# Kernel optimization log

Hardware: AMD Instinct MI355X
Metric: run time of the kernel (lower is better)

Reference implementation:

```python
import jax, jax.numpy as jnp
import numpy as np

U, N, E, D = 200000, 50000, 1600000, 64


def setup_inputs() -> dict:
    key = jax.random.key(0)
    ks = jax.random.split(key, 8)
    nodes = jax.random.randint(ks[0], (N,), 0, U)
    neigh_idx = jax.random.randint(ks[1], (E,), 0, U)
    seg_ids = jnp.sort(jax.random.randint(ks[2], (E,), 0, N))
    u2e = jax.random.normal(ks[3], (U, D), dtype=jnp.float32) * 0.1
    W1 = jax.random.normal(ks[4], (2 * D, D), dtype=jnp.float32) * 0.1
    b1 = jnp.zeros((D,), dtype=jnp.float32)
    W2 = jax.random.normal(ks[5], (D, D), dtype=jnp.float32) * 0.1
    b2 = jnp.zeros((D,), dtype=jnp.float32)
    w3 = jax.random.normal(ks[6], (D, 1), dtype=jnp.float32) * 0.1
    b3 = jnp.zeros((1,), dtype=jnp.float32)
    return {"nodes": nodes, "neigh_idx": neigh_idx, "seg_ids": seg_ids,
            "u2e": u2e, "W1": W1, "b1": b1, "W2": W2, "b2": b2,
            "w3": w3, "b3": b3}


def reference(nodes, neigh_idx, seg_ids, u2e, W1, b1, W2, b2, w3, b3):
    # Per-node self representation  [N, D]
    u_rep = u2e[nodes]
    # Ragged neighbor gather flattened to edge list
    e_u = u2e[neigh_idx]                      # [E, D]
    u_edge = u_rep[seg_ids]                   # [E, D] node rep broadcast to its edges
    # Attention MLP (GraphRec-style), eval mode (no dropout)
    x = jnp.concatenate([e_u, u_edge], axis=1)            # [E, 2D]
    x = jax.nn.relu(x @ W1 + b1)
    x = jax.nn.relu(x @ W2 + b2)
    logits = (x @ w3 + b3)[:, 0]                           # [E]
    # Segment softmax over each node's neighbor set
    seg_max = jax.ops.segment_max(logits, seg_ids, num_segments=N)
    ex = jnp.exp(logits - seg_max[seg_ids])
    denom = jax.ops.segment_sum(ex, seg_ids, num_segments=N)
    att = ex / denom[seg_ids]                              # [E]
    # Attention-weighted neighbor aggregation: e_u^T @ att per node
    agg = jax.ops.segment_sum(att[:, None] * e_u, seg_ids, num_segments=N)  # [N, D]
    # Nodes with zero neighbors fall back to their own embedding
    counts = jax.ops.segment_sum(jnp.ones((E,), dtype=jnp.float32), seg_ids, num_segments=N)
    out = jnp.where(counts[:, None] > 0, agg, u_rep)
    return out
```

## Files before the change

kernel.cpp:

```cpp
#include <hip/hip_runtime.h>
#include <math.h>

#define D 64

typedef __fp16 fp16x2 __attribute__((ext_vector_type(2)));
typedef _Float16 half8 __attribute__((ext_vector_type(8)));
typedef _Float16 half4v __attribute__((ext_vector_type(4)));
typedef __attribute__((ext_vector_type(4))) float f32x4;

union h8pun { half8 v; fp16x2 h2[4]; };

__global__ __launch_bounds__(256) void k_prep(const float* __restrict__ W1,
                                              const float* __restrict__ W2,
                                              float* __restrict__ W1at,
                                              float* __restrict__ W1bt,
                                              _Float16* __restrict__ W2h,
                                              const int* __restrict__ seg_ids,
                                              int* __restrict__ start, int E, int N) {
    int i = blockIdx.x * 256 + threadIdx.x;
    if (i < 3 * D * D) {
        int mat = i / (D * D), j = i % (D * D);
        if (mat == 0) {
            int r = j >> 6, c = j & 63;
            W1at[c * D + r] = W1[r * D + c];
        } else if (mat == 1) {
            int r = j >> 6, c = j & 63;
            W1bt[c * D + r] = W1[(D + r) * D + c];
        } else {
            int n = j >> 6, pos = j & 63;
            int k = (pos >> 2) + 16 * (pos & 3);
            W2h[n * D + pos] = (_Float16)W2[k * D + n];
        }
    }
    if (i <= N) {
        int lo = 0, hi = E;
        while (lo < hi) {
            int mid = (lo + hi) >> 1;
            if (seg_ids[mid] < i) lo = mid + 1; else hi = mid;
        }
        start[i] = lo;
    }
}

__global__ __launch_bounds__(256) void k_proj_both(const float* __restrict__ u2e,
                                                   const int* __restrict__ nodes,
                                                   const float* __restrict__ W1at,
                                                   const float* __restrict__ W1bt,
                                                   const float* __restrict__ b1,
                                                   _Float16* __restrict__ q,
                                                   _Float16* __restrict__ u2e_h,
                                                   _Float16* __restrict__ p,
                                                   int U, int N, int wavesU, int wavesN) {
    int lane = threadIdx.x & 63;
    int m = lane & 15, quad = lane >> 4;
    int wave = (blockIdx.x * blockDim.x + threadIdx.x) >> 6;

    const float* Wt;
    const int* idx;
    const float* bias;
    _Float16* outp;
    _Float16* copyp;
    int R, w0, wstride;
    if (wave < wavesU) {
        Wt = W1at; idx = nullptr; bias = nullptr; outp = q; copyp = u2e_h;
        R = U; w0 = wave; wstride = wavesU;
    } else {
        Wt = W1bt; idx = nodes; bias = b1; outp = p; copyp = nullptr;
        R = N; w0 = wave - wavesU; wstride = wavesN;
    }

    half8 Bf[2][4];
    float bv[4];
#pragma unroll
    for (int t = 0; t < 4; ++t) {
        int n = m + 16 * t;
        bv[t] = bias ? bias[n] : 0.0f;
#pragma unroll
        for (int kh = 0; kh < 2; ++kh) {
            const float* col = Wt + n * D + kh * 32 + quad * 8;
#pragma unroll
            for (int j = 0; j < 8; ++j) Bf[kh][t][j] = (_Float16)col[j];
        }
    }

    int ngroups = (R + 15) / 16;
    for (int g = w0; g < ngroups; g += wstride) {
        int r_ = g * 16 + m;
        int rs = r_ < R ? r_ : R - 1;
        int src = idx ? idx[rs] : rs;
        const float4* arow = (const float4*)(u2e + (size_t)src * D);
        float4 x0 = arow[quad * 2], x1 = arow[quad * 2 + 1];
        float4 y0 = arow[8 + quad * 2], y1 = arow[8 + quad * 2 + 1];
        h8pun A0, A1;
        A0.h2[0] = __builtin_amdgcn_cvt_pkrtz(x0.x, x0.y);
        A0.h2[1] = __builtin_amdgcn_cvt_pkrtz(x0.z, x0.w);
        A0.h2[2] = __builtin_amdgcn_cvt_pkrtz(x1.x, x1.y);
        A0.h2[3] = __builtin_amdgcn_cvt_pkrtz(x1.z, x1.w);
        A1.h2[0] = __builtin_amdgcn_cvt_pkrtz(y0.x, y0.y);
        A1.h2[1] = __builtin_amdgcn_cvt_pkrtz(y0.z, y0.w);
        A1.h2[2] = __builtin_amdgcn_cvt_pkrtz(y1.x, y1.y);
        A1.h2[3] = __builtin_amdgcn_cvt_pkrtz(y1.z, y1.w);
        if (copyp && r_ < R) {
            *(half8*)(copyp + (size_t)r_ * D + quad * 8) = A0.v;
            *(half8*)(copyp + (size_t)r_ * D + 32 + quad * 8) = A1.v;
        }
        f32x4 C[4];
#pragma unroll
        for (int t = 0; t < 4; ++t) C[t] = (f32x4){bv[t], bv[t], bv[t], bv[t]};
#pragma unroll
        for (int t = 0; t < 4; ++t) {
            C[t] = __builtin_amdgcn_mfma_f32_16x16x32_f16(A0.v, Bf[0][t], C[t], 0, 0, 0);
            C[t] = __builtin_amdgcn_mfma_f32_16x16x32_f16(A1.v, Bf[1][t], C[t], 0, 0, 0);
        }
#pragma unroll
        for (int r = 0; r < 4; ++r) {
            int row = g * 16 + quad * 4 + r;
            if (row < R) {
                half4v hv = {(_Float16)C[0][r], (_Float16)C[1][r],
                             (_Float16)C[2][r], (_Float16)C[3][r]};
                *(half4v*)(outp + (size_t)row * D + m * 4) = hv;
            }
        }
    }
}

__global__ __launch_bounds__(256) void k_edge_ex(const int* __restrict__ neigh_idx,
                                                 const int* __restrict__ seg_ids,
                                                 const _Float16* __restrict__ q,
                                                 const _Float16* __restrict__ p,
                                                 const _Float16* __restrict__ W2h,
                                                 const float* __restrict__ b2,
                                                 const float* __restrict__ w3,
                                                 const float* __restrict__ b3,
                                                 float* __restrict__ exb, int E) {
    int lane = threadIdx.x & 63;
    int m = lane & 15, quad = lane >> 4;

    half8 Bf[2][4];
    float b2v[4], w3v[4];
#pragma unroll
    for (int t = 0; t < 4; ++t) {
        int n = m + 16 * t;
        b2v[t] = b2[n];
        w3v[t] = w3[n];
        Bf[0][t] = *(const half8*)(W2h + n * D + quad * 8);
        Bf[1][t] = *(const half8*)(W2h + n * D + 32 + quad * 8);
    }
    float b3v = b3[0];
    const half8 hz = {0, 0, 0, 0, 0, 0, 0, 0};

    int ngroups = (E + 31) / 32;
    int wave = (blockIdx.x * blockDim.x + threadIdx.x) >> 6;
    int nwaves = (gridDim.x * blockDim.x) >> 6;
    for (int g = wave; g < ngroups; g += nwaves) {
        int ea = g * 32 + m, eb = ea + 16;
        int eas = ea < E ? ea : E - 1;
        int ebs = eb < E ? eb : E - 1;
        int nbra = neigh_idx[eas], sega = seg_ids[eas];
        int nbrb = neigh_idx[ebs], segb = seg_ids[ebs];
        const half8* qra = (const half8*)(q + (size_t)nbra * D);
        const half8* pra = (const half8*)(p + (size_t)sega * D);
        const half8* qrb = (const half8*)(q + (size_t)nbrb * D);
        const half8* prb = (const half8*)(p + (size_t)segb * D);
        half8 qa0 = qra[quad], qa1 = qra[quad + 4];
        half8 pa0 = pra[quad], pa1 = pra[quad + 4];
        half8 qb0 = qrb[quad], qb1 = qrb[quad + 4];
        half8 pb0 = prb[quad], pb1 = prb[quad + 4];
        half8 Aa0 = __builtin_elementwise_max(qa0 + pa0, hz);
        half8 Aa1 = __builtin_elementwise_max(qa1 + pa1, hz);
        half8 Ab0 = __builtin_elementwise_max(qb0 + pb0, hz);
        half8 Ab1 = __builtin_elementwise_max(qb1 + pb1, hz);
        f32x4 Ca[4], Cb[4];
#pragma unroll
        for (int t = 0; t < 4; ++t) {
            Ca[t] = (f32x4){b2v[t], b2v[t], b2v[t], b2v[t]};
            Cb[t] = Ca[t];
        }
#pragma unroll
        for (int t = 0; t < 4; ++t) {
            Ca[t] = __builtin_amdgcn_mfma_f32_16x16x32_f16(Aa0, Bf[0][t], Ca[t], 0, 0, 0);
            Ca[t] = __builtin_amdgcn_mfma_f32_16x16x32_f16(Aa1, Bf[1][t], Ca[t], 0, 0, 0);
            Cb[t] = __builtin_amdgcn_mfma_f32_16x16x32_f16(Ab0, Bf[0][t], Cb[t], 0, 0, 0);
            Cb[t] = __builtin_amdgcn_mfma_f32_16x16x32_f16(Ab1, Bf[1][t], Cb[t], 0, 0, 0);
        }
        float pa[4], pb[4];
#pragma unroll
        for (int r = 0; r < 4; ++r) {
            float sa = 0.0f, sb = 0.0f;
#pragma unroll
            for (int t = 0; t < 4; ++t) {
                sa += fmaxf(Ca[t][r], 0.0f) * w3v[t];
                sb += fmaxf(Cb[t][r], 0.0f) * w3v[t];
            }
            pa[r] = sa; pb[r] = sb;
        }
#pragma unroll
        for (int off = 1; off <= 8; off <<= 1) {
#pragma unroll
            for (int r = 0; r < 4; ++r) {
                pa[r] += __shfl_xor(pa[r], off, 64);
                pb[r] += __shfl_xor(pb[r], off, 64);
            }
        }
        if (m == 0) {
            int e0 = g * 32 + quad * 4;
            if (e0 + 3 < E)
                *(float4*)(exb + e0) = make_float4(__expf(pa[0] + b3v), __expf(pa[1] + b3v),
                                                   __expf(pa[2] + b3v), __expf(pa[3] + b3v));
            else
#pragma unroll
                for (int r = 0; r < 4; ++r)
                    if (e0 + r < E) exb[e0 + r] = __expf(pa[r] + b3v);
            int e1 = e0 + 16;
            if (e1 + 3 < E)
                *(float4*)(exb + e1) = make_float4(__expf(pb[0] + b3v), __expf(pb[1] + b3v),
                                                   __expf(pb[2] + b3v), __expf(pb[3] + b3v));
            else
#pragma unroll
                for (int r = 0; r < 4; ++r)
                    if (e1 + r < E) exb[e1 + r] = __expf(pb[r] + b3v);
        }
    }
}

__global__ __launch_bounds__(256) void k_agg_fast(const int* __restrict__ nodes,
                                                  const int* __restrict__ neigh_idx,
                                                  const float* __restrict__ u2e,
                                                  const _Float16* __restrict__ u2e_h,
                                                  const float* __restrict__ exb,
                                                  const int* __restrict__ start,
                                                  float* __restrict__ out, int N) {
    int n = blockIdx.x * 4 + ((int)threadIdx.x >> 6);
    int lane = threadIdx.x & 63;
    if (n >= N) return;
    int s = start[n];
    int t = start[n + 1];
    if (s == t) {
        int node = nodes[n];
        out[(size_t)n * D + lane] = u2e[(size_t)node * D + lane];
        return;
    }

    int grp = lane >> 3, sub = lane & 7;
    float acc[8];
#pragma unroll
    for (int j = 0; j < 8; ++j) acc[j] = 0.0f;
    float dsum = 0.0f;
    for (int i = s; i < t; i += 32) {
#pragma unroll
        for (int uu = 0; uu < 4; ++uu) {
            int ii = i + uu * 8 + grp;
            bool v = ii < t;
            int is = v ? ii : s;
            float w = exb[is];
            int nb = neigh_idx[is];
            half8 r = *(const half8*)(u2e_h + (size_t)nb * D + sub * 8);
            if (!v) w = 0.0f;
            dsum += w;
#pragma unroll
            for (int j = 0; j < 8; ++j) acc[j] += w * (float)r[j];
        }
    }
#pragma unroll
    for (int off = 8; off <= 32; off <<= 1) {
#pragma unroll
        for (int j = 0; j < 8; ++j) acc[j] += __shfl_xor(acc[j], off, 64);
        dsum += __shfl_xor(dsum, off, 64);
    }
    if (grp == 0) {
        float inv = 1.0f / dsum;
        float* o = out + (size_t)n * D + sub * 8;
        *(float4*)o = make_float4(acc[0] * inv, acc[1] * inv, acc[2] * inv, acc[3] * inv);
        *(float4*)(o + 4) = make_float4(acc[4] * inv, acc[5] * inv, acc[6] * inv, acc[7] * inv);
    }
}

extern "C" void kernel_launch(void* const* d_in, const int* in_sizes, int n_in,
                              void* d_out, int out_size, void* d_ws, size_t ws_size,
                              hipStream_t stream) {
    const int* nodes = (const int*)d_in[0];
    const int* neigh_idx = (const int*)d_in[1];
    const int* seg_ids = (const int*)d_in[2];
    const float* u2e = (const float*)d_in[3];
    const float* W1 = (const float*)d_in[4];
    const float* b1 = (const float*)d_in[5];
    const float* W2 = (const float*)d_in[6];
    const float* b2 = (const float*)d_in[7];
    const float* w3 = (const float*)d_in[8];
    const float* b3 = (const float*)d_in[9];
    float* out = (float*)d_out;

    int N = in_sizes[0];
    int E = in_sizes[1];
    int U = in_sizes[3] / D;

    char* ws = (char*)d_ws;
    size_t off = 0;
    auto alloc = [&](size_t bytes) {
        void* ptr = ws + off;
        off = (off + bytes + 255) & ~(size_t)255;
        return ptr;
    };
    float* exb = (float*)alloc((size_t)E * 4);
    int* start = (int*)alloc((size_t)(N + 1) * 4);
    float* W1at = (float*)alloc((size_t)D * D * 4);
    float* W1bt = (float*)alloc((size_t)D * D * 4);
    _Float16* W2h = (_Float16*)alloc((size_t)D * D * 2);
    _Float16* q = (_Float16*)alloc((size_t)U * D * 2);
    _Float16* p = (_Float16*)alloc((size_t)N * D * 2);
    _Float16* u2e_h = (_Float16*)alloc((size_t)U * D * 2);
    (void)ws_size;

    int prep_n = (N + 1) > 3 * D * D ? (N + 1) : 3 * D * D;
    k_prep<<<(prep_n + 255) / 256, 256, 0, stream>>>(W1, W2, W1at, W1bt, W2h,
                                                     seg_ids, start, E, N);
    const int wavesU = 6144, wavesN = 2048;
    k_proj_both<<<(wavesU + wavesN) / 4, 256, 0, stream>>>(u2e, nodes, W1at, W1bt, b1,
                                                           q, u2e_h, p, U, N, wavesU, wavesN);
    k_edge_ex<<<2048, 256, 0, stream>>>(neigh_idx, seg_ids, q, p, W2h,
                                        b2, w3, b3, exb, E);
    k_agg_fast<<<(N + 3) / 4, 256, 0, stream>>>(nodes, neigh_idx, u2e, u2e_h,
                                                exb, start, out, N);
}
```

Before: 223.1 us.

## Fuse edge scoring and aggregation per edge chunk with boundary partials

Merges the edge-logit kernel and the per-node aggregation kernel into one kernel. Each wave handles a contiguous 128-edge chunk, keeps its exp values and neighbor indices in LDS, and aggregates the segments that fall inside the chunk directly. Segments that cross a chunk boundary write partial sums to slots, and a new finish kernel combines them and handles empty nodes. This removes the global exb round trip and the reload of neighbor indices, at the cost of one extra launch and a per-element finish pass. Softmax is still computed without max subtraction, as before.

```diff
diff --git a/kernel.cpp b/kernel.cpp
--- a/kernel.cpp
+++ b/kernel.cpp
@@ -2,6 +2,7 @@
 #include <math.h>
 
 #define D 64
+#define CHUNK 128
 
 typedef __fp16 fp16x2 __attribute__((ext_vector_type(2)));
 typedef _Float16 half8 __attribute__((ext_vector_type(8)));
@@ -16,7 +17,9 @@
                                               float* __restrict__ W1bt,
                                               _Float16* __restrict__ W2h,
                                               const int* __restrict__ seg_ids,
-                                              int* __restrict__ start, int E, int N) {
+                                              int* __restrict__ start,
+                                              int* __restrict__ pnode,
+                                              int E, int N, int nslots) {
     int i = blockIdx.x * 256 + threadIdx.x;
     if (i < 3 * D * D) {
         int mat = i / (D * D), j = i % (D * D);
@@ -40,6 +43,7 @@
         }
         start[i] = lo;
     }
+    if (i < nslots) pnode[i] = -1;
 }
 
 __global__ __launch_bounds__(256) void k_proj_both(const float* __restrict__ u2e,
@@ -124,36 +128,52 @@
     }
 }
 
-__global__ __launch_bounds__(256) void k_edge_ex(const int* __restrict__ neigh_idx,
-                                                 const int* __restrict__ seg_ids,
-                                                 const _Float16* __restrict__ q,
-                                                 const _Float16* __restrict__ p,
-                                                 const _Float16* __restrict__ W2h,
-                                                 const float* __restrict__ b2,
-                                                 const float* __restrict__ w3,
-                                                 const float* __restrict__ b3,
-                                                 float* __restrict__ exb, int E) {
+__global__ __launch_bounds__(256) void k_fused(const int* __restrict__ neigh_idx,
+                                               const int* __restrict__ seg_ids,
+                                               const _Float16* __restrict__ q,
+                                               const _Float16* __restrict__ p,
+                                               const _Float16* __restrict__ u2e_h,
+                                               const _Float16* __restrict__ W2h,
+                                               const float* __restrict__ b2,
+                                               const float* __restrict__ w3,
+                                               const float* __restrict__ b3,
+                                               const int* __restrict__ start,
+                                               float* __restrict__ out,
+                                               int* __restrict__ pnode,
+                                               float* __restrict__ pdenom,
+                                               float* __restrict__ pacc,
+                                               int E, int nchunks) {
+    __shared__ float lds_ex[4][CHUNK];
+    __shared__ int lds_nb[4][CHUNK];
+    int wib = (int)threadIdx.x >> 6;
+    float* lex = lds_ex[wib];
+    int* lnb = lds_nb[wib];
+
     int lane = threadIdx.x & 63;
     int m = lane & 15, quad = lane >> 4;
+    int wave = (blockIdx.x * blockDim.x + threadIdx.x) >> 6;
+    if (wave >= nchunks) return;
+    int e_beg = wave * CHUNK;
+    int e_end = e_beg + CHUNK;
+    if (e_end > E) e_end = E;
 
     half8 Bf[2][4];
     float b2v[4], w3v[4];
 #pragma unroll
     for (int t = 0; t < 4; ++t) {
-        int n = m + 16 * t;
-        b2v[t] = b2[n];
-        w3v[t] = w3[n];
-        Bf[0][t] = *(const half8*)(W2h + n * D + quad * 8);
-        Bf[1][t] = *(const half8*)(W2h + n * D + 32 + quad * 8);
+        int nn = m + 16 * t;
+        b2v[t] = b2[nn];
+        w3v[t] = w3[nn];
+        Bf[0][t] = *(const half8*)(W2h + nn * D + quad * 8);
+        Bf[1][t] = *(const half8*)(W2h + nn * D + 32 + quad * 8);
     }
     float b3v = b3[0];
     const half8 hz = {0, 0, 0, 0, 0, 0, 0, 0};
 
-    int ngroups = (E + 31) / 32;
-    int wave = (blockIdx.x * blockDim.x + threadIdx.x) >> 6;
-    int nwaves = (gridDim.x * blockDim.x) >> 6;
-    for (int g = wave; g < ngroups; g += nwaves) {
-        int ea = g * 32 + m, eb = ea + 16;
+    int nit = (e_end - e_beg + 31) >> 5;
+    for (int g = 0; g < nit; ++g) {
+        int base = e_beg + g * 32;
+        int ea = base + m, eb = ea + 16;
         int eas = ea < E ? ea : E - 1;
         int ebs = eb < E ? eb : E - 1;
         int nbra = neigh_idx[eas], sega = seg_ids[eas];
@@ -203,76 +223,103 @@
             }
         }
         if (m == 0) {
-            int e0 = g * 32 + quad * 4;
-            if (e0 + 3 < E)
-                *(float4*)(exb + e0) = make_float4(__expf(pa[0] + b3v), __expf(pa[1] + b3v),
-                                                   __expf(pa[2] + b3v), __expf(pa[3] + b3v));
-            else
-#pragma unroll
-                for (int r = 0; r < 4; ++r)
-                    if (e0 + r < E) exb[e0 + r] = __expf(pa[r] + b3v);
-            int e1 = e0 + 16;
-            if (e1 + 3 < E)
-                *(float4*)(exb + e1) = make_float4(__expf(pb[0] + b3v), __expf(pb[1] + b3v),
-                                                   __expf(pb[2] + b3v), __expf(pb[3] + b3v));
-            else
-#pragma unroll
-                for (int r = 0; r < 4; ++r)
-                    if (e1 + r < E) exb[e1 + r] = __expf(pb[r] + b3v);
-        }
-    }
-}
-
-__global__ __launch_bounds__(256) void k_agg_fast(const int* __restrict__ nodes,
-                                                  const int* __restrict__ neigh_idx,
-                                                  const float* __restrict__ u2e,
-                                                  const _Float16* __restrict__ u2e_h,
-                                                  const float* __restrict__ exb,
-                                                  const int* __restrict__ start,
-                                                  float* __restrict__ out, int N) {
-    int n = blockIdx.x * 4 + ((int)threadIdx.x >> 6);
-    int lane = threadIdx.x & 63;
-    if (n >= N) return;
-    int s = start[n];
-    int t = start[n + 1];
-    if (s == t) {
-        int node = nodes[n];
-        out[(size_t)n * D + lane] = u2e[(size_t)node * D + lane];
+            int o0 = g * 32 + quad * 4;
+            *(float4*)(lex + o0) = make_float4(__expf(pa[0] + b3v), __expf(pa[1] + b3v),
+                                               __expf(pa[2] + b3v), __expf(pa[3] + b3v));
+            *(float4*)(lex + o0 + 16) = make_float4(__expf(pb[0] + b3v), __expf(pb[1] + b3v),
+                                                    __expf(pb[2] + b3v), __expf(pb[3] + b3v));
+        }
+        if (quad == 0) {
+            lnb[g * 32 + m] = nbra;
+            lnb[g * 32 + 16 + m] = nbrb;
+        }
+    }
+
+    int n0 = seg_ids[e_beg];
+    int n1 = seg_ids[e_end - 1];
+    int grp = lane >> 3, sub = lane & 7;
+    for (int n = n0; n <= n1; ++n) {
+        int sf = start[n], tf = start[n + 1];
+        int s = sf > e_beg ? sf : e_beg;
+        int t = tf < e_end ? tf : e_end;
+        if (s >= t) continue;
+        float acc[8];
+#pragma unroll
+        for (int j = 0; j < 8; ++j) acc[j] = 0.0f;
+        float dsum = 0.0f;
+        for (int i = s; i < t; i += 32) {
+#pragma unroll
+            for (int uu = 0; uu < 4; ++uu) {
+                int ii = i + uu * 8 + grp;
+                bool v = ii < t;
+                int li = (v ? ii : s) - e_beg;
+                float w = lex[li];
+                int nb = lnb[li];
+                half8 r = *(const half8*)(u2e_h + (size_t)nb * D + sub * 8);
+                if (!v) w = 0.0f;
+                dsum += w;
+#pragma unroll
+                for (int j = 0; j < 8; ++j) acc[j] += w * (float)r[j];
+            }
+        }
+#pragma unroll
+        for (int off = 8; off <= 32; off <<= 1) {
+#pragma unroll
+            for (int j = 0; j < 8; ++j) acc[j] += __shfl_xor(acc[j], off, 64);
+            dsum += __shfl_xor(dsum, off, 64);
+        }
+        bool interior = (sf >= e_beg) && (tf <= e_end);
+        if (interior) {
+            if (grp == 0) {
+                float inv = 1.0f / dsum;
+                float* o = out + (size_t)n * D + sub * 8;
+                *(float4*)o = make_float4(acc[0] * inv, acc[1] * inv, acc[2] * inv, acc[3] * inv);
+                *(float4*)(o + 4) = make_float4(acc[4] * inv, acc[5] * inv, acc[6] * inv, acc[7] * inv);
+            }
+        } else {
+            int slot = wave * 2 + (sf < e_beg ? 0 : 1);
+            if (grp == 0) {
+                float* pa_ = pacc + (size_t)slot * D + sub * 8;
+                *(float4*)pa_ = make_float4(acc[0], acc[1], acc[2], acc[3]);
+                *(float4*)(pa_ + 4) = make_float4(acc[4], acc[5], acc[6], acc[7]);
+            }
+            if (lane == 0) {
+                pdenom[slot] = dsum;
+                pnode[slot] = n;
+            }
+        }
+    }
+}
+
+__global__ __launch_bounds__(256) void k_finish(const int* __restrict__ nodes,
+                                                const float* __restrict__ u2e,
+                                                const int* __restrict__ start,
+                                                const int* __restrict__ pnode,
+                                                const float* __restrict__ pdenom,
+                                                const float* __restrict__ pacc,
+                                                float* __restrict__ out, int N) {
+    int i = blockIdx.x * 256 + threadIdx.x;
+    if (i >= N * D) return;
+    int n = i >> 6, d = i & 63;
+    int sf = start[n], tf = start[n + 1];
+    if (sf == tf) {
+        out[i] = u2e[(size_t)nodes[n] * D + d];
         return;
     }
-
-    int grp = lane >> 3, sub = lane & 7;
-    float acc[8];
-#pragma unroll
-    for (int j = 0; j < 8; ++j) acc[j] = 0.0f;
-    float dsum = 0.0f;
-    for (int i = s; i < t; i += 32) {
-#pragma unroll
-        for (int uu = 0; uu < 4; ++uu) {
-            int ii = i + uu * 8 + grp;
-            bool v = ii < t;
-            int is = v ? ii : s;
-            float w = exb[is];
-            int nb = neigh_idx[is];
-            half8 r = *(const half8*)(u2e_h + (size_t)nb * D + sub * 8);
-            if (!v) w = 0.0f;
-            dsum += w;
-#pragma unroll
-            for (int j = 0; j < 8; ++j) acc[j] += w * (float)r[j];
-        }
-    }
-#pragma unroll
-    for (int off = 8; off <= 32; off <<= 1) {
-#pragma unroll
-        for (int j = 0; j < 8; ++j) acc[j] += __shfl_xor(acc[j], off, 64);
-        dsum += __shfl_xor(dsum, off, 64);
-    }
-    if (grp == 0) {
-        float inv = 1.0f / dsum;
-        float* o = out + (size_t)n * D + sub * 8;
-        *(float4*)o = make_float4(acc[0] * inv, acc[1] * inv, acc[2] * inv, acc[3] * inv);
-        *(float4*)(o + 4) = make_float4(acc[4] * inv, acc[5] * inv, acc[6] * inv, acc[7] * inv);
-    }
+    int wlo = sf / CHUNK, whi = (tf - 1) / CHUNK;
+    if (wlo == whi) return;
+    float acc = 0.0f, dsum = 0.0f;
+    for (int w = wlo; w <= whi; ++w) {
+#pragma unroll
+        for (int sl = 0; sl < 2; ++sl) {
+            int idx = w * 2 + sl;
+            if (pnode[idx] == n) {
+                acc += pacc[(size_t)idx * D + d];
+                dsum += pdenom[idx];
+            }
+        }
+    }
+    out[i] = acc / dsum;
 }
 
 extern "C" void kernel_launch(void* const* d_in, const int* in_sizes, int n_in,
@@ -294,6 +341,9 @@
     int E = in_sizes[1];
     int U = in_sizes[3] / D;
 
+    int nchunks = (E + CHUNK - 1) / CHUNK;
+    int nslots = nchunks * 2;
+
     char* ws = (char*)d_ws;
     size_t off = 0;
     auto alloc = [&](size_t bytes) {
@@ -301,7 +351,6 @@
         off = (off + bytes + 255) & ~(size_t)255;
         return ptr;
     };
-    float* exb = (float*)alloc((size_t)E * 4);
     int* start = (int*)alloc((size_t)(N + 1) * 4);
     float* W1at = (float*)alloc((size_t)D * D * 4);
     float* W1bt = (float*)alloc((size_t)D * D * 4);
@@ -309,16 +358,21 @@
     _Float16* q = (_Float16*)alloc((size_t)U * D * 2);
     _Float16* p = (_Float16*)alloc((size_t)N * D * 2);
     _Float16* u2e_h = (_Float16*)alloc((size_t)U * D * 2);
+    int* pnode = (int*)alloc((size_t)nslots * 4);
+    float* pdenom = (float*)alloc((size_t)nslots * 4);
+    float* pacc = (float*)alloc((size_t)nslots * D * 4);
     (void)ws_size;
 
     int prep_n = (N + 1) > 3 * D * D ? (N + 1) : 3 * D * D;
+    if (prep_n < nslots) prep_n = nslots;
     k_prep<<<(prep_n + 255) / 256, 256, 0, stream>>>(W1, W2, W1at, W1bt, W2h,
-                                                     seg_ids, start, E, N);
+                                                     seg_ids, start, pnode, E, N, nslots);
     const int wavesU = 6144, wavesN = 2048;
     k_proj_both<<<(wavesU + wavesN) / 4, 256, 0, stream>>>(u2e, nodes, W1at, W1bt, b1,
                                                            q, u2e_h, p, U, N, wavesU, wavesN);
-    k_edge_ex<<<2048, 256, 0, stream>>>(neigh_idx, seg_ids, q, p, W2h,
-                                        b2, w3, b3, exb, E);
-    k_agg_fast<<<(N + 3) / 4, 256, 0, stream>>>(nodes, neigh_idx, u2e, u2e_h,
-                                                exb, start, out, N);
-}
+    k_fused<<<(nchunks + 3) / 4, 256, 0, stream>>>(neigh_idx, seg_ids, q, p, u2e_h,
+                                                   W2h, b2, w3, b3, start, out,
+                                                   pnode, pdenom, pacc, E, nchunks);
+    k_finish<<<(N * D + 255) / 256, 256, 0, stream>>>(nodes, u2e, start, pnode,
+                                                      pdenom, pacc, out, N);
+}
```

Result: slower. 240.4 us (+7.8%).

## Fold prep kernel into projection kernel and prefetch next edge indices

Applied to the files above, without the earlier changes.

Removes the separate k_prep launch. The segment-start binary search and the W2 fp16 permutation now run inside k_proj_both, and W1 is read directly with strided loads instead of through transposed copies. The edge kernel also software-pipelines its loop by loading the next group's neighbor and segment indices before working on the current group, hiding index-load latency. This saves one launch and the W1 transpose buffers, at the cost of uncoalesced W1 reads per wave and a few extra registers in the edge loop.

```diff
diff --git a/kernel.cpp b/kernel.cpp
--- a/kernel.cpp
+++ b/kernel.cpp
@@ -10,63 +10,49 @@
 
 union h8pun { half8 v; fp16x2 h2[4]; };
 
-__global__ __launch_bounds__(256) void k_prep(const float* __restrict__ W1,
-                                              const float* __restrict__ W2,
-                                              float* __restrict__ W1at,
-                                              float* __restrict__ W1bt,
-                                              _Float16* __restrict__ W2h,
-                                              const int* __restrict__ seg_ids,
-                                              int* __restrict__ start, int E, int N) {
-    int i = blockIdx.x * 256 + threadIdx.x;
-    if (i < 3 * D * D) {
-        int mat = i / (D * D), j = i % (D * D);
-        if (mat == 0) {
-            int r = j >> 6, c = j & 63;
-            W1at[c * D + r] = W1[r * D + c];
-        } else if (mat == 1) {
-            int r = j >> 6, c = j & 63;
-            W1bt[c * D + r] = W1[(D + r) * D + c];
-        } else {
-            int n = j >> 6, pos = j & 63;
-            int k = (pos >> 2) + 16 * (pos & 3);
-            W2h[n * D + pos] = (_Float16)W2[k * D + n];
-        }
-    }
-    if (i <= N) {
+__global__ __launch_bounds__(256) void k_proj_both(const float* __restrict__ u2e,
+                                                   const int* __restrict__ nodes,
+                                                   const float* __restrict__ W1,
+                                                   const float* __restrict__ b1,
+                                                   const float* __restrict__ W2,
+                                                   _Float16* __restrict__ W2h,
+                                                   const int* __restrict__ seg_ids,
+                                                   int* __restrict__ start,
+                                                   _Float16* __restrict__ q,
+                                                   _Float16* __restrict__ u2e_h,
+                                                   _Float16* __restrict__ p,
+                                                   int U, int N, int E,
+                                                   int wavesU, int wavesN) {
+    int tid = blockIdx.x * blockDim.x + (int)threadIdx.x;
+    if (tid <= N) {
         int lo = 0, hi = E;
         while (lo < hi) {
             int mid = (lo + hi) >> 1;
-            if (seg_ids[mid] < i) lo = mid + 1; else hi = mid;
-        }
-        start[i] = lo;
-    }
-}
-
-__global__ __launch_bounds__(256) void k_proj_both(const float* __restrict__ u2e,
-                                                   const int* __restrict__ nodes,
-                                                   const float* __restrict__ W1at,
-                                                   const float* __restrict__ W1bt,
-                                                   const float* __restrict__ b1,
-                                                   _Float16* __restrict__ q,
-                                                   _Float16* __restrict__ u2e_h,
-                                                   _Float16* __restrict__ p,
-                                                   int U, int N, int wavesU, int wavesN) {
+            if (seg_ids[mid] < tid) lo = mid + 1; else hi = mid;
+        }
+        start[tid] = lo;
+    } else if (tid <= N + D * D) {
+        int j = tid - (N + 1);
+        int n = j >> 6, pos = j & 63;
+        int k = (pos >> 2) + 16 * (pos & 3);
+        W2h[n * D + pos] = (_Float16)W2[k * D + n];
+    }
+
     int lane = threadIdx.x & 63;
     int m = lane & 15, quad = lane >> 4;
     int wave = (blockIdx.x * blockDim.x + threadIdx.x) >> 6;
 
-    const float* Wt;
     const int* idx;
     const float* bias;
     _Float16* outp;
     _Float16* copyp;
-    int R, w0, wstride;
+    int R, w0, wstride, w1off;
     if (wave < wavesU) {
-        Wt = W1at; idx = nullptr; bias = nullptr; outp = q; copyp = u2e_h;
-        R = U; w0 = wave; wstride = wavesU;
+        idx = nullptr; bias = nullptr; outp = q; copyp = u2e_h;
+        R = U; w0 = wave; wstride = wavesU; w1off = 0;
     } else {
-        Wt = W1bt; idx = nodes; bias = b1; outp = p; copyp = nullptr;
-        R = N; w0 = wave - wavesU; wstride = wavesN;
+        idx = nodes; bias = b1; outp = p; copyp = nullptr;
+        R = N; w0 = wave - wavesU; wstride = wavesN; w1off = D;
     }
 
     half8 Bf[2][4];
@@ -77,9 +63,9 @@
         bv[t] = bias ? bias[n] : 0.0f;
 #pragma unroll
         for (int kh = 0; kh < 2; ++kh) {
-            const float* col = Wt + n * D + kh * 32 + quad * 8;
-#pragma unroll
-            for (int j = 0; j < 8; ++j) Bf[kh][t][j] = (_Float16)col[j];
+            int k0 = w1off + kh * 32 + quad * 8;
+#pragma unroll
+            for (int j = 0; j < 8; ++j) Bf[kh][t][j] = (_Float16)W1[(size_t)(k0 + j) * D + n];
         }
     }
 
@@ -152,12 +138,25 @@
     int ngroups = (E + 31) / 32;
     int wave = (blockIdx.x * blockDim.x + threadIdx.x) >> 6;
     int nwaves = (gridDim.x * blockDim.x) >> 6;
-    for (int g = wave; g < ngroups; g += nwaves) {
-        int ea = g * 32 + m, eb = ea + 16;
+
+    int nbra = 0, sega = 0, nbrb = 0, segb = 0;
+    if (wave < ngroups) {
+        int ea = wave * 32 + m, eb = ea + 16;
         int eas = ea < E ? ea : E - 1;
         int ebs = eb < E ? eb : E - 1;
-        int nbra = neigh_idx[eas], sega = seg_ids[eas];
-        int nbrb = neigh_idx[ebs], segb = seg_ids[ebs];
+        nbra = neigh_idx[eas]; sega = seg_ids[eas];
+        nbrb = neigh_idx[ebs]; segb = seg_ids[ebs];
+    }
+    for (int g = wave; g < ngroups; g += nwaves) {
+        int gn = g + nwaves;
+        int nbra_n = 0, sega_n = 0, nbrb_n = 0, segb_n = 0;
+        if (gn < ngroups) {
+            int ea = gn * 32 + m, eb = ea + 16;
+            int eas = ea < E ? ea : E - 1;
+            int ebs = eb < E ? eb : E - 1;
+            nbra_n = neigh_idx[eas]; sega_n = seg_ids[eas];
+            nbrb_n = neigh_idx[ebs]; segb_n = seg_ids[ebs];
+        }
         const half8* qra = (const half8*)(q + (size_t)nbra * D);
         const half8* pra = (const half8*)(p + (size_t)sega * D);
         const half8* qrb = (const half8*)(q + (size_t)nbrb * D);
@@ -220,6 +219,7 @@
                 for (int r = 0; r < 4; ++r)
                     if (e1 + r < E) exb[e1 + r] = __expf(pb[r] + b3v);
         }
+        nbra = nbra_n; sega = sega_n; nbrb = nbrb_n; segb = segb_n;
     }
 }
 
@@ -303,20 +303,16 @@
     };
     float* exb = (float*)alloc((size_t)E * 4);
     int* start = (int*)alloc((size_t)(N + 1) * 4);
-    float* W1at = (float*)alloc((size_t)D * D * 4);
-    float* W1bt = (float*)alloc((size_t)D * D * 4);
     _Float16* W2h = (_Float16*)alloc((size_t)D * D * 2);
     _Float16* q = (_Float16*)alloc((size_t)U * D * 2);
     _Float16* p = (_Float16*)alloc((size_t)N * D * 2);
     _Float16* u2e_h = (_Float16*)alloc((size_t)U * D * 2);
     (void)ws_size;
 
-    int prep_n = (N + 1) > 3 * D * D ? (N + 1) : 3 * D * D;
-    k_prep<<<(prep_n + 255) / 256, 256, 0, stream>>>(W1, W2, W1at, W1bt, W2h,
-                                                     seg_ids, start, E, N);
     const int wavesU = 6144, wavesN = 2048;
-    k_proj_both<<<(wavesU + wavesN) / 4, 256, 0, stream>>>(u2e, nodes, W1at, W1bt, b1,
-                                                           q, u2e_h, p, U, N, wavesU, wavesN);
+    k_proj_both<<<(wavesU + wavesN) / 4, 256, 0, stream>>>(u2e, nodes, W1, b1, W2, W2h,
+                                                           seg_ids, start, q, u2e_h, p,
+                                                           U, N, E, wavesU, wavesN);
     k_edge_ex<<<2048, 256, 0, stream>>>(neigh_idx, seg_ids, q, p, W2h,
                                         b2, w3, b3, exb, E);
     k_agg_fast<<<(N + 3) / 4, 256, 0, stream>>>(nodes, neigh_idx, u2e, u2e_h,
```

After: 209.6 us (median of 2 runs). 1.06x faster.
